# Performance work log

Measured on AMD Instinct MI355X. Metric: run time of the kernel, lower is better.

Reference implementation:

```python
import jax, jax.numpy as jnp
import numpy as np

N_VAR = 1_000_000
N_CON = 500_000
N_EDGE = 8_000_000
H = 10  # n_h_feats


def setup_inputs() -> dict:
    key = jax.random.key(0)
    ks = jax.random.split(key, 20)
    f32 = jnp.float32
    s = 0.3  # weight init scale
    return {
        'var_c': jax.random.normal(ks[0], (N_VAR,), f32),
        'var_x': jax.random.normal(ks[1], (N_VAR,), f32),
        'con_b': jax.random.normal(ks[2], (N_CON,), f32),
        'edge_src': jax.random.randint(ks[3], (N_EDGE,), 0, N_VAR, jnp.int32),
        'edge_dst': jax.random.randint(ks[4], (N_EDGE,), 0, N_CON, jnp.int32),
        'edge_w': jax.random.uniform(ks[5], (N_EDGE,), f32),
        'Wv': jax.random.normal(ks[6], (2, H), f32) * s,
        'bv': jnp.zeros((H,), f32),
        'Wc': jax.random.normal(ks[7], (1, H), f32) * s,
        'bc': jnp.zeros((H,), f32),
        'W1': jax.random.normal(ks[8], (H, H), f32) * s,
        'b1': jnp.zeros((H,), f32),
        'W2': jax.random.normal(ks[9], (H, H), f32) * s,
        'b2': jnp.zeros((H,), f32),
        'Wo1': jax.random.normal(ks[10], (H, H), f32) * s,
        'bo1': jnp.zeros((H,), f32),
        'Wo2': jax.random.normal(ks[11], (H, H), f32) * s,
        'bo2': jnp.zeros((H,), f32),
        'Wo3': jax.random.normal(ks[12], (H, 1), f32) * s,
        'bo3': jnp.zeros((1,), f32),
    }


def _graph_conv(feat_src, src, dst, w, n_dst, deg_src, deg_dst, W, b):
    # DGL GraphConv, norm='both', with edge weights:
    # h = D_src^{-1/2} x ; m_e = h[src_e] * w_e ; agg = scatter_sum(m, dst)
    # out = (D_dst^{-1/2} agg) @ W + b
    h = feat_src * jax.lax.rsqrt(deg_src)[:, None]
    m = h[src] * w[:, None]                      # [E, H] gather + scale
    agg = jax.ops.segment_sum(m, dst, num_segments=n_dst)  # scatter-add
    agg = agg * jax.lax.rsqrt(deg_dst)[:, None]
    return agg @ W + b


def reference(var_c, var_x, con_b, edge_src, edge_dst, edge_w,
              Wv, bv, Wc, bc, W1, b1, W2, b2, Wo1, bo1, Wo2, bo2, Wo3, bo3):
    # node embeddings
    var_feat = jnp.stack([var_c, var_x], axis=1)            # [N_VAR, 2]
    con_feat = con_b.reshape(-1, 1)                          # [N_CON, 1]
    X_var = jax.nn.relu(var_feat @ Wv + bv)                  # [N_VAR, H]
    X_con = jax.nn.relu(con_feat @ Wc + bc)                  # computed in original; unused by GraphConv (no dst-feat term)

    ones_e = jnp.ones((edge_src.shape[0],), jnp.float32)
    deg_var = jnp.maximum(jax.ops.segment_sum(ones_e, edge_src, num_segments=N_VAR), 1.0)
    deg_con = jnp.maximum(jax.ops.segment_sum(ones_e, edge_dst, num_segments=N_CON), 1.0)

    # conv1['con'] is overwritten by conv2['con'] in the original (v2c src feats are X_var both times)
    h_con = jax.nn.relu(_graph_conv(X_var, edge_src, edge_dst, edge_w, N_CON, deg_var, deg_con, W2, b2))
    # likewise conv1['var'] is overwritten by conv2['var'] (c2v src feats are h_con both times)
    h_var = jax.nn.relu(_graph_conv(h_con, edge_dst, edge_src, edge_w, N_VAR, deg_con, deg_var, W2, b2))

    z = jax.nn.relu(h_var @ Wo1 + bo1)
    z = jax.nn.relu(z @ Wo2 + bo2)
    logit = z @ Wo3 + bo3                                    # [N_VAR, 1]
    # dgl.readout_nodes(op='mean') over a single batched graph
    return jnp.mean(logit, axis=0, keepdims=True)            # [1, 1]
```

## Files before the change

### kernel.cpp

```cpp
#include <hip/hip_runtime.h>

#define NVAR 1000000
#define NCON 500000
#define EPB 8192
#define FCAP 4480


__global__ __launch_bounds__(256) void kA_hist2(const int4* __restrict__ src4,
                                                const int4* __restrict__ dst4,
                                                unsigned* __restrict__ bhV,
                                                unsigned* __restrict__ bhC,
                                                int ne4, int nblk) {
    __shared__ unsigned hv[1024], hc[1024];
    int tid = threadIdx.x, b = blockIdx.x;
    for (int t = tid; t < 1024; t += 256) { hv[t] = 0; hc[t] = 0; }
    __syncthreads();
    int beg = b * (EPB / 4), end = min(ne4, beg + (EPB / 4));
    for (int i = beg + tid; i < end; i += 256) {
        int4 s = src4[i];
        int4 d = dst4[i];
        atomicAdd(&hv[s.x >> 10], 1u); atomicAdd(&hv[s.y >> 10], 1u);
        atomicAdd(&hv[s.z >> 10], 1u); atomicAdd(&hv[s.w >> 10], 1u);
        atomicAdd(&hc[d.x >> 9], 1u);  atomicAdd(&hc[d.y >> 9], 1u);
        atomicAdd(&hc[d.z >> 9], 1u);  atomicAdd(&hc[d.w >> 9], 1u);
    }
    __syncthreads();
    for (int t = tid; t < 1024; t += 256) {
        bhV[(size_t)t * nblk + b] = hv[t];
        bhC[(size_t)t * nblk + b] = hc[t];
    }
}

__global__ __launch_bounds__(256) void kA_scat(const int* __restrict__ keys,
                                               const int* __restrict__ vals,
                                               const float* __restrict__ w,
                                               const unsigned int* __restrict__ scanned,
                                               int2* __restrict__ bucketed,
                                               int ne, int shift, int nblk) {
    __shared__ unsigned int h[1024];
    __shared__ unsigned int lb[1024];
    __shared__ unsigned int gb[1024];
    __shared__ unsigned int sc[256];
    __shared__ int2 stage[EPB];
    int tid = threadIdx.x, b = blockIdx.x;
    for (int t = tid; t < 1024; t += 256) {
        h[t] = 0;
        gb[t] = scanned[(size_t)t * nblk + b];
    }
    __syncthreads();
    int beg = b * EPB, end = min(ne, beg + EPB), cnt = end - beg;
    int cnt4 = cnt >> 2;
    const int4* keys4 = (const int4*)(keys + beg);
    for (int i = tid; i < cnt4; i += 256) {
        int4 k = keys4[i];
        atomicAdd(&h[k.x >> shift], 1u);
        atomicAdd(&h[k.y >> shift], 1u);
        atomicAdd(&h[k.z >> shift], 1u);
        atomicAdd(&h[k.w >> shift], 1u);
    }
    for (int i = cnt4 * 4 + tid; i < cnt; i += 256) atomicAdd(&h[keys[beg + i] >> shift], 1u);
    __syncthreads();
    unsigned v0, v1, v2, v3;
    int q = tid * 4;
    v0 = h[q]; v1 = h[q + 1]; v2 = h[q + 2]; v3 = h[q + 3];
    sc[tid] = v0 + v1 + v2 + v3;
    __syncthreads();
    for (int dd = 1; dd < 256; dd <<= 1) {
        unsigned add = (tid >= dd) ? sc[tid - dd] : 0u;
        __syncthreads();
        sc[tid] += add;
        __syncthreads();
    }
    unsigned ex = (tid == 0) ? 0u : sc[tid - 1];
    lb[q]     = ex;
    lb[q + 1] = ex + v0;
    lb[q + 2] = ex + v0 + v1;
    lb[q + 3] = ex + v0 + v1 + v2;
    __syncthreads();
    for (int t = tid; t < 1024; t += 256) h[t] = 0;
    __syncthreads();
    unsigned mask = (1u << shift) - 1u;
    const int4* vals4 = (const int4*)(vals + beg);
    const float4* w4 = (const float4*)(w + beg);
    for (int i = tid; i < cnt4; i += 256) {
        int4 k = keys4[i];
        int4 v = vals4[i];
        float4 ww = w4[i];
        {
            unsigned bkt = (unsigned)k.x >> shift;
            unsigned r = atomicAdd(&h[bkt], 1u);
            stage[lb[bkt] + r] = make_int2(__float_as_int(ww.x),
                                           (v.x << shift) | (unsigned)(k.x & (int)mask));
        }
        {
            unsigned bkt = (unsigned)k.y >> shift;
            unsigned r = atomicAdd(&h[bkt], 1u);
            stage[lb[bkt] + r] = make_int2(__float_as_int(ww.y),
                                           (v.y << shift) | (unsigned)(k.y & (int)mask));
        }
        {
            unsigned bkt = (unsigned)k.z >> shift;
            unsigned r = atomicAdd(&h[bkt], 1u);
            stage[lb[bkt] + r] = make_int2(__float_as_int(ww.z),
                                           (v.z << shift) | (unsigned)(k.z & (int)mask));
        }
        {
            unsigned bkt = (unsigned)k.w >> shift;
            unsigned r = atomicAdd(&h[bkt], 1u);
            stage[lb[bkt] + r] = make_int2(__float_as_int(ww.w),
                                           (v.w << shift) | (unsigned)(k.w & (int)mask));
        }
    }
    for (int i = cnt4 * 4 + tid; i < cnt; i += 256) {
        int k = keys[beg + i];
        unsigned bkt = (unsigned)k >> shift;
        unsigned r = atomicAdd(&h[bkt], 1u);
        stage[lb[bkt] + r] = make_int2(__float_as_int(w[beg + i]),
                                       (vals[beg + i] << shift) | (unsigned)(k & (int)mask));
    }
    __syncthreads();
    for (int i = tid; i < cnt; i += 256) {
        unsigned bb = 0;
#pragma unroll
        for (int step = 512; step > 0; step >>= 1) {
            unsigned cand = bb + step;
            if (cand < 1024 && lb[cand] <= (unsigned)i) bb = cand;
        }
        bucketed[gb[bb] + ((unsigned)i - lb[bb])] = stage[i];
    }
}

__global__ __launch_bounds__(256) void kB_degV(const int2* __restrict__ bucketed,
                                               const unsigned* __restrict__ scanned,
                                               unsigned* __restrict__ deg,
                                               int nnodes, int nblk) {
    __shared__ unsigned h[1024];
    int d = blockIdx.x, tid = threadIdx.x;
    unsigned base = scanned[(size_t)d * nblk], next = scanned[(size_t)(d + 1) * nblk];
    for (int t = tid; t < 1024; t += 256) h[t] = 0;
    __syncthreads();
    for (unsigned i = base + tid; i < next; i += 256)
        atomicAdd(&h[(unsigned)bucketed[i].y & 1023u], 1u);
    __syncthreads();
    int lo = d << 10;
    for (int t = tid; t < 1024; t += 256) {
        int node = lo + t;
        if (node < nnodes) deg[node] = h[t];
    }
}

__global__ __launch_bounds__(256) void k_scan_blocks(const unsigned int* __restrict__ in,
                                                     unsigned int* __restrict__ out,
                                                     unsigned int* __restrict__ bsum,
                                                     int n) {
    __shared__ unsigned int sT[256];
    int base = blockIdx.x * 1024 + threadIdx.x * 4;
    unsigned int v0 = 0, v1 = 0, v2 = 0, v3 = 0;
    if (base + 3 < n) {
        uint4 u = *(const uint4*)(in + base);
        v0 = u.x; v1 = u.y; v2 = u.z; v3 = u.w;
    } else {
        if (base     < n) v0 = in[base];
        if (base + 1 < n) v1 = in[base + 1];
        if (base + 2 < n) v2 = in[base + 2];
        if (base + 3 < n) v3 = in[base + 3];
    }
    sT[threadIdx.x] = v0 + v1 + v2 + v3;
    __syncthreads();
    for (int d = 1; d < 256; d <<= 1) {
        unsigned int add = (threadIdx.x >= (unsigned)d) ? sT[threadIdx.x - d] : 0u;
        __syncthreads();
        sT[threadIdx.x] += add;
        __syncthreads();
    }
    unsigned int excl = (threadIdx.x == 0) ? 0u : sT[threadIdx.x - 1];
    if (base     < n) out[base]     = excl;
    if (base + 1 < n) out[base + 1] = excl + v0;
    if (base + 2 < n) out[base + 2] = excl + v0 + v1;
    if (base + 3 < n) out[base + 3] = excl + v0 + v1 + v2;
    if (threadIdx.x == 255 && bsum) bsum[blockIdx.x] = sT[255];
}

__global__ __launch_bounds__(256) void k_scan_add(unsigned int* __restrict__ data,
                                                  const unsigned int* __restrict__ bscan,
                                                  int n) {
    int base = blockIdx.x * 1024 + threadIdx.x * 4;
    unsigned int add = bscan[blockIdx.x];
    if (base + 3 < n) {
        uint4 u = *(const uint4*)(data + base);
        u.x += add; u.y += add; u.z += add; u.w += add;
        *(uint4*)(data + base) = u;
    } else {
        if (base     < n) data[base]     += add;
        if (base + 1 < n) data[base + 1] += add;
        if (base + 2 < n) data[base + 2] += add;
        if (base + 3 < n) data[base + 3] += add;
    }
}


__global__ __launch_bounds__(256) void k_xvar_p(const float* __restrict__ var_c,
                                                const float* __restrict__ var_x,
                                                const unsigned int* __restrict__ deg_var,
                                                const float* __restrict__ Wv,
                                                const float* __restrict__ bv,
                                                float* __restrict__ Xs, int n) {
    int i = blockIdx.x * blockDim.x + threadIdx.x;
    if (i >= n) return;
    float c = var_c[i], x = var_x[i];
    float rs = rsqrtf(fmaxf((float)deg_var[i], 1.0f));
    float o[16];
#pragma unroll
    for (int j = 0; j < 10; j++) {
        float t = fmaf(c, Wv[j], fmaf(x, Wv[10 + j], bv[j]));
        o[j] = fmaxf(t, 0.0f) * rs;
    }
#pragma unroll
    for (int j = 10; j < 16; j++) o[j] = 0.0f;
    float4* dst4 = (float4*)(Xs + (size_t)i * 16);
#pragma unroll
    for (int j = 0; j < 4; j++)
        dst4[j] = make_float4(o[4 * j], o[4 * j + 1], o[4 * j + 2], o[4 * j + 3]);
}

#define GATHER4(eA, eB, eC, eD, TAB)                                          \
    {                                                                         \
        float4 v0 = *(const float4*)(TAB + (size_t)(eA).y * 16 + c0);         \
        float4 v1 = *(const float4*)(TAB + (size_t)(eB).y * 16 + c0);         \
        float4 v2 = *(const float4*)(TAB + (size_t)(eC).y * 16 + c0);         \
        float4 v3 = *(const float4*)(TAB + (size_t)(eD).y * 16 + c0);         \
        float w0 = __int_as_float((eA).x), w1 = __int_as_float((eB).x);       \
        float w2 = __int_as_float((eC).x), w3 = __int_as_float((eD).x);       \
        acc.x = fmaf(w0, v0.x, acc.x); acc.y = fmaf(w0, v0.y, acc.y);         \
        acc.z = fmaf(w0, v0.z, acc.z); acc.w = fmaf(w0, v0.w, acc.w);         \
        acc.x = fmaf(w1, v1.x, acc.x); acc.y = fmaf(w1, v1.y, acc.y);         \
        acc.z = fmaf(w1, v1.z, acc.z); acc.w = fmaf(w1, v1.w, acc.w);         \
        acc.x = fmaf(w2, v2.x, acc.x); acc.y = fmaf(w2, v2.y, acc.y);         \
        acc.z = fmaf(w2, v2.z, acc.z); acc.w = fmaf(w2, v2.w, acc.w);         \
        acc.x = fmaf(w3, v3.x, acc.x); acc.y = fmaf(w3, v3.y, acc.y);         \
        acc.z = fmaf(w3, v3.z, acc.z); acc.w = fmaf(w3, v3.w, acc.w);         \
    }

__global__ __launch_bounds__(512) void kF_con(const int2* __restrict__ bucketed,
                                              const unsigned* __restrict__ scanned,
                                              const float* __restrict__ Xs,
                                              const float* __restrict__ W2,
                                              const float* __restrict__ b2,
                                              float* __restrict__ hs, int nblk) {
    __shared__ unsigned h[512], s[512], tmp[512];
    __shared__ float sW[100], sb[10];
    __shared__ int2 stage[FCAP];
    int tid = threadIdx.x;
    int d = blockIdx.x >> 1, half = blockIdx.x & 1;
    for (int t = tid; t < 100; t += 512) sW[t] = W2[t];
    if (tid < 10) sb[tid] = b2[tid];
    h[tid] = 0;
    __syncthreads();
    unsigned base = scanned[(size_t)d * nblk];
    unsigned next = scanned[(size_t)(d + 1) * nblk];
    int bsz = (int)(next - base);
    for (int i = tid; i < bsz; i += 512)
        atomicAdd(&h[(unsigned)bucketed[base + i].y & 511u], 1u);
    __syncthreads();
    unsigned hv = h[tid];
    tmp[tid] = hv;
    __syncthreads();
    for (int dd = 1; dd < 512; dd <<= 1) {
        unsigned add = (tid >= dd) ? tmp[tid - dd] : 0u;
        __syncthreads();
        tmp[tid] += add;
        __syncthreads();
    }
    s[tid] = tmp[tid] - hv;
    __syncthreads();
    int hb = half * 256;
    unsigned own_beg = s[hb];
    unsigned own_end = (hb + 256 == 512) ? (unsigned)bsz : s[hb + 256];
    bool fit = (int)(own_end - own_beg) <= FCAP;
    h[tid] = 0;
    __syncthreads();
    if (fit) {
        for (int i = tid; i < bsz; i += 512) {
            int2 p = bucketed[base + i];
            unsigned low = (unsigned)p.y & 511u;
            if ((int)(low >> 8) == half) {
                unsigned r = atomicAdd(&h[low], 1u);
                stage[s[low] + r - own_beg] = make_int2(p.x, p.y >> 9);
            }
        }
    }
    __syncthreads();
    int quad = tid >> 2, lane = tid & 3, c0 = lane * 4;
#pragma unroll
    for (int rr = 0; rr < 2; rr++) {
        int node = hb + rr * 128 + quad;
        int g = (d << 9) + node;
        if (g >= NCON) continue;
        float4 acc = make_float4(0.f, 0.f, 0.f, 0.f);
        unsigned cnt;
        if (fit) {
            unsigned beg = s[node] - own_beg;
            cnt = h[node];
            unsigned end = beg + cnt, p = beg;
            for (; p + 4 <= end; p += 4) {
                int2 e0 = stage[p], e1 = stage[p + 1], e2 = stage[p + 2], e3 = stage[p + 3];
                GATHER4(e0, e1, e2, e3, Xs);
            }
            for (; p < end; ++p) {
                int2 e = stage[p];
                float4 v = *(const float4*)(Xs + (size_t)e.y * 16 + c0);
                float we = __int_as_float(e.x);
                acc.x = fmaf(we, v.x, acc.x); acc.y = fmaf(we, v.y, acc.y);
                acc.z = fmaf(we, v.z, acc.z); acc.w = fmaf(we, v.w, acc.w);
            }
        } else {
            cnt = 0;
            for (int i = 0; i < bsz; ++i) {
                int2 p = bucketed[base + i];
                if (((unsigned)p.y & 511u) == (unsigned)node) {
                    ++cnt;
                    float4 v = *(const float4*)(Xs + (size_t)((unsigned)p.y >> 9) * 16 + c0);
                    float we = __int_as_float(p.x);
                    acc.x = fmaf(we, v.x, acc.x); acc.y = fmaf(we, v.y, acc.y);
                    acc.z = fmaf(we, v.z, acc.z); acc.w = fmaf(we, v.w, acc.w);
                }
            }
        }
        float rs = rsqrtf(fmaxf((float)cnt, 1.0f));
        float a[10];
        a[0] = __shfl(acc.x, 0, 4); a[1] = __shfl(acc.y, 0, 4);
        a[2] = __shfl(acc.z, 0, 4); a[3] = __shfl(acc.w, 0, 4);
        a[4] = __shfl(acc.x, 1, 4); a[5] = __shfl(acc.y, 1, 4);
        a[6] = __shfl(acc.z, 1, 4); a[7] = __shfl(acc.w, 1, 4);
        a[8] = __shfl(acc.x, 2, 4); a[9] = __shfl(acc.y, 2, 4);
#pragma unroll
        for (int j = 0; j < 10; j++) a[j] *= rs;
        float o[12];
#pragma unroll
        for (int k = 0; k < 10; k++) {
            float t = sb[k];
#pragma unroll
            for (int j = 0; j < 10; j++) t = fmaf(a[j], sW[j * 10 + k], t);
            o[k] = fmaxf(t, 0.0f) * rs;
        }
        o[10] = 0.0f; o[11] = 0.0f;
        float4 wv = (lane < 3) ? make_float4(o[c0], o[c0 + 1], o[c0 + 2], o[c0 + 3])
                               : make_float4(0.f, 0.f, 0.f, 0.f);
        *(float4*)(hs + (size_t)g * 16 + c0) = wv;
    }
}

__global__ __launch_bounds__(512) void kF_fin(const int2* __restrict__ bucketed,
                                              const unsigned* __restrict__ scanned,
                                              const float* __restrict__ feat,
                                              const float* __restrict__ W2,
                                              const float* __restrict__ b2,
                                              const float* __restrict__ Wo1,
                                              const float* __restrict__ bo1,
                                              const float* __restrict__ Wo2,
                                              const float* __restrict__ bo2,
                                              const float* __restrict__ Wo3,
                                              const float* __restrict__ bo3,
                                              double* __restrict__ partials, int nblk) {
    __shared__ unsigned h[1024], s[1024], tmp[512];
    __shared__ float sW2[100], sb2[10], sWo1[100], sbo1[10], sWo2[100], sbo2[10], sWo3[10], sbo3v;
    __shared__ int2 stage[FCAP];
    __shared__ double red[512];
    int tid = threadIdx.x;
    int d = blockIdx.x >> 1, half = blockIdx.x & 1;
    for (int t = tid; t < 100; t += 512) { sW2[t] = W2[t]; sWo1[t] = Wo1[t]; sWo2[t] = Wo2[t]; }
    if (tid < 10) {
        sb2[tid] = b2[tid]; sbo1[tid] = bo1[tid]; sbo2[tid] = bo2[tid]; sWo3[tid] = Wo3[tid];
    }
    if (tid == 0) sbo3v = bo3[0];
    h[tid] = 0; h[tid + 512] = 0;
    __syncthreads();
    unsigned base = scanned[(size_t)d * nblk];
    unsigned next = scanned[(size_t)(d + 1) * nblk];
    int bsz = (int)(next - base);
    for (int i = tid; i < bsz; i += 512)
        atomicAdd(&h[(unsigned)bucketed[base + i].y & 1023u], 1u);
    __syncthreads();
    int q = tid * 2;
    unsigned v0 = h[q], v1 = h[q + 1];
    tmp[tid] = v0 + v1;
    __syncthreads();
    for (int dd = 1; dd < 512; dd <<= 1) {
        unsigned add = (tid >= dd) ? tmp[tid - dd] : 0u;
        __syncthreads();
        tmp[tid] += add;
        __syncthreads();
    }
    unsigned excl = tmp[tid] - (v0 + v1);
    s[q] = excl; s[q + 1] = excl + v0;
    __syncthreads();
    int hb = half * 512;
    unsigned own_beg = s[hb];
    unsigned own_end = (hb + 512 == 1024) ? (unsigned)bsz : s[hb + 512];
    bool fit = (int)(own_end - own_beg) <= FCAP;
    h[tid] = 0; h[tid + 512] = 0;
    __syncthreads();
    if (fit) {
        for (int i = tid; i < bsz; i += 512) {
            int2 p = bucketed[base + i];
            unsigned low = (unsigned)p.y & 1023u;
            if ((int)(low >> 9) == half) {
                unsigned r = atomicAdd(&h[low], 1u);
                stage[s[low] + r - own_beg] = make_int2(p.x, p.y >> 10);
            }
        }
    }
    __syncthreads();
    int quad = tid >> 2, lane = tid & 3, c0 = lane * 4;
    double accd = 0.0;
#pragma unroll
    for (int rr = 0; rr < 4; rr++) {
        int node = hb + rr * 128 + quad;
        int g = (d << 10) + node;
        if (g >= NVAR) continue;
        float4 acc = make_float4(0.f, 0.f, 0.f, 0.f);
        unsigned cnt;
        if (fit) {
            unsigned beg = s[node] - own_beg;
            cnt = h[node];
            unsigned end = beg + cnt, p = beg;
            for (; p + 4 <= end; p += 4) {
                int2 e0 = stage[p], e1 = stage[p + 1], e2 = stage[p + 2], e3 = stage[p + 3];
                GATHER4(e0, e1, e2, e3, feat);
            }
            for (; p < end; ++p) {
                int2 e = stage[p];
                float4 v = *(const float4*)(feat + (size_t)e.y * 16 + c0);
                float we = __int_as_float(e.x);
                acc.x = fmaf(we, v.x, acc.x); acc.y = fmaf(we, v.y, acc.y);
                acc.z = fmaf(we, v.z, acc.z); acc.w = fmaf(we, v.w, acc.w);
            }
        } else {
            cnt = 0;
            for (int i = 0; i < bsz; ++i) {
                int2 p = bucketed[base + i];
                if (((unsigned)p.y & 1023u) == (unsigned)node) {
                    ++cnt;
                    float4 v = *(const float4*)(feat + (size_t)((unsigned)p.y >> 10) * 16 + c0);
                    float we = __int_as_float(p.x);
                    acc.x = fmaf(we, v.x, acc.x); acc.y = fmaf(we, v.y, acc.y);
                    acc.z = fmaf(we, v.z, acc.z); acc.w = fmaf(we, v.w, acc.w);
                }
            }
        }
        float rs = rsqrtf(fmaxf((float)cnt, 1.0f));
        float a[10];
        a[0] = __shfl(acc.x, 0, 4); a[1] = __shfl(acc.y, 0, 4);
        a[2] = __shfl(acc.z, 0, 4); a[3] = __shfl(acc.w, 0, 4);
        a[4] = __shfl(acc.x, 1, 4); a[5] = __shfl(acc.y, 1, 4);
        a[6] = __shfl(acc.z, 1, 4); a[7] = __shfl(acc.w, 1, 4);
        a[8] = __shfl(acc.x, 2, 4); a[9] = __shfl(acc.y, 2, 4);
#pragma unroll
        for (int j = 0; j < 10; j++) a[j] *= rs;
        float hh[10], z[10];
#pragma unroll
        for (int k = 0; k < 10; k++) {
            float t = sb2[k];
#pragma unroll
            for (int j = 0; j < 10; j++) t = fmaf(a[j], sW2[j * 10 + k], t);
            hh[k] = fmaxf(t, 0.0f);
        }
#pragma unroll
        for (int k = 0; k < 10; k++) {
            float t = sbo1[k];
#pragma unroll
            for (int j = 0; j < 10; j++) t = fmaf(hh[j], sWo1[j * 10 + k], t);
            z[k] = fmaxf(t, 0.0f);
        }
        float t3 = sbo3v;
#pragma unroll
        for (int k = 0; k < 10; k++) {
            float t = sbo2[k];
#pragma unroll
            for (int j = 0; j < 10; j++) t = fmaf(z[j], sWo2[j * 10 + k], t);
            t = fmaxf(t, 0.0f);
            t3 = fmaf(t, sWo3[k], t3);
        }
        if (lane == 0) accd += (double)t3;
    }
    red[tid] = accd;
    __syncthreads();
    for (int off = 256; off > 0; off >>= 1) {
        if (tid < off) red[tid] += red[tid + off];
        __syncthreads();
    }
    if (tid == 0) partials[blockIdx.x] = red[0];
}

__global__ __launch_bounds__(256) void k_out(const double* __restrict__ partials, int np,
                                             float* __restrict__ out) {
    __shared__ double red[256];
    double a = 0.0;
    for (int i = threadIdx.x; i < np; i += blockDim.x) a += partials[i];
    red[threadIdx.x] = a;
    __syncthreads();
    for (int off = 128; off > 0; off >>= 1) {
        if (threadIdx.x < off) red[threadIdx.x] += red[threadIdx.x + off];
        __syncthreads();
    }
    if (threadIdx.x == 0) out[0] = (float)(red[0] / (double)NVAR);
}


extern "C" void kernel_launch(void* const* d_in, const int* in_sizes, int n_in,
                              void* d_out, int out_size, void* d_ws, size_t ws_size,
                              hipStream_t stream) {
    const float* var_c  = (const float*)d_in[0];
    const float* var_x  = (const float*)d_in[1];
    const int*   e_src  = (const int*)d_in[3];
    const int*   e_dst  = (const int*)d_in[4];
    const float* e_w    = (const float*)d_in[5];
    const float* Wv     = (const float*)d_in[6];
    const float* bv     = (const float*)d_in[7];
    const float* W2     = (const float*)d_in[12];
    const float* b2     = (const float*)d_in[13];
    const float* Wo1    = (const float*)d_in[14];
    const float* bo1    = (const float*)d_in[15];
    const float* Wo2    = (const float*)d_in[16];
    const float* bo2    = (const float*)d_in[17];
    const float* Wo3    = (const float*)d_in[18];
    const float* bo3    = (const float*)d_in[19];
    float* out = (float*)d_out;
    const int ne = in_sizes[3];
    (void)n_in; (void)out_size; (void)ws_size;

    const int B = 256;
    const int nblkA = (ne + EPB - 1) / EPB;
    const int scanN = 1024 * nblkA;
    const int NBs   = (scanN + 1023) / 1024;
    const int BKV   = (NVAR + 1023) >> 10;
    const int BKC   = (NCON + 511) >> 9;
    const int ne4   = ne / 4;

    char* ws = (char*)d_ws;
    size_t off = 0;
    auto walloc = [&](size_t bytes) {
        void* p = ws + off;
        off = (off + bytes + 255) & ~(size_t)255;
        return p;
    };

    int2*     bucketedV = (int2*)walloc((size_t)ne * 8);
    int2*     bucketedC = (int2*)walloc((size_t)ne * 8);
    float*    Xs64      = (float*)walloc((size_t)NVAR * 16 * 4);
    float*    hs64      = (float*)walloc((size_t)NCON * 16 * 4);
    unsigned* scannedV  = (unsigned*)walloc((size_t)scanN * 4);
    unsigned* scannedC  = (unsigned*)walloc((size_t)scanN * 4);
    unsigned* bhV       = (unsigned*)walloc((size_t)scanN * 4);
    unsigned* bhC       = (unsigned*)walloc((size_t)scanN * 4);
    unsigned* bsumV     = (unsigned*)walloc(4096);
    unsigned* bscanV    = (unsigned*)walloc(4096);
    unsigned* bsumC     = (unsigned*)walloc(4096);
    unsigned* bscanC    = (unsigned*)walloc(4096);
    unsigned* bdummy    = (unsigned*)walloc(256);
    unsigned* deg_var   = bhV;
    double*   partials  = (double*)bhC;

    kA_hist2<<<nblkA, B, 0, stream>>>((const int4*)e_src, (const int4*)e_dst,
                                      bhV, bhC, ne4, nblkA);

    k_scan_blocks<<<NBs, B, 0, stream>>>(bhV, scannedV, bsumV, scanN);
    k_scan_blocks<<<1,   B, 0, stream>>>(bsumV, bscanV, bdummy, NBs);
    k_scan_add   <<<NBs, B, 0, stream>>>(scannedV, bscanV, scanN);
    k_scan_blocks<<<NBs, B, 0, stream>>>(bhC, scannedC, bsumC, scanN);
    k_scan_blocks<<<1,   B, 0, stream>>>(bsumC, bscanC, bdummy, NBs);
    k_scan_add   <<<NBs, B, 0, stream>>>(scannedC, bscanC, scanN);

    kA_scat<<<nblkA, B, 0, stream>>>(e_src, e_dst, e_w, scannedV, bucketedV, ne, 10, nblkA);

    kB_degV<<<BKV, B, 0, stream>>>(bucketedV, scannedV, deg_var, NVAR, nblkA);

    k_xvar_p<<<(NVAR + B - 1) / B, B, 0, stream>>>(var_c, var_x, deg_var, Wv, bv, Xs64, NVAR);

    kA_scat<<<nblkA, B, 0, stream>>>(e_dst, e_src, e_w, scannedC, bucketedC, ne, 9, nblkA);

    kF_con<<<BKC * 2, 512, 0, stream>>>(bucketedC, scannedC, Xs64, W2, b2, hs64, nblkA);

    kF_fin<<<BKV * 2, 512, 0, stream>>>(bucketedV, scannedV, hs64, W2, b2,
                                        Wo1, bo1, Wo2, bo2, Wo3, bo3, partials, nblkA);

    k_out<<<1, B, 0, stream>>>(partials, BKV * 2, out);
}
```

Baseline: 580.0 us.

## Precompute per-node degree prefix sums globally instead of per-block histogram and scan

```diff
diff --git a/kernel.cpp b/kernel.cpp
--- a/kernel.cpp
+++ b/kernel.cpp
@@ -130,28 +130,30 @@
     }
 }
 
-__global__ __launch_bounds__(256) void kB_degV(const int2* __restrict__ bucketed,
-                                               const unsigned* __restrict__ scanned,
-                                               unsigned* __restrict__ deg,
-                                               int nnodes, int nblk) {
+__global__ __launch_bounds__(256) void kDeg(const int2* __restrict__ bucketed,
+                                            const unsigned* __restrict__ scanned,
+                                            unsigned* __restrict__ deg,
+                                            int nnodes, int nblk, int lowbits) {
     __shared__ unsigned h[1024];
     int d = blockIdx.x, tid = threadIdx.x;
+    int W = 1 << lowbits;
+    unsigned mask = (unsigned)(W - 1);
     unsigned base = scanned[(size_t)d * nblk], next = scanned[(size_t)(d + 1) * nblk];
-    for (int t = tid; t < 1024; t += 256) h[t] = 0;
+    for (int t = tid; t < W; t += 256) h[t] = 0;
     __syncthreads();
     for (unsigned i = base + tid; i < next; i += 256)
-        atomicAdd(&h[(unsigned)bucketed[i].y & 1023u], 1u);
-    __syncthreads();
-    int lo = d << 10;
-    for (int t = tid; t < 1024; t += 256) {
+        atomicAdd(&h[(unsigned)bucketed[i].y & mask], 1u);
+    __syncthreads();
+    int lo = d << lowbits;
+    for (int t = tid; t < W; t += 256) {
         int node = lo + t;
         if (node < nnodes) deg[node] = h[t];
     }
 }
 
-__global__ __launch_bounds__(256) void k_scan_blocks(const unsigned int* __restrict__ in,
-                                                     unsigned int* __restrict__ out,
-                                                     unsigned int* __restrict__ bsum,
+__global__ __launch_bounds__(256) void k_scan_blocks(const unsigned int* in,
+                                                     unsigned int* out,
+                                                     unsigned int* bsum,
                                                      int n) {
     __shared__ unsigned int sT[256];
     int base = blockIdx.x * 1024 + threadIdx.x * 4;
@@ -243,49 +245,38 @@
 
 __global__ __launch_bounds__(512) void kF_con(const int2* __restrict__ bucketed,
                                               const unsigned* __restrict__ scanned,
+                                              const unsigned* __restrict__ startC,
                                               const float* __restrict__ Xs,
                                               const float* __restrict__ W2,
                                               const float* __restrict__ b2,
-                                              float* __restrict__ hs, int nblk) {
-    __shared__ unsigned h[512], s[512], tmp[512];
+                                              float* __restrict__ hs, int nblk, int netot) {
+    __shared__ unsigned sraw[257], cr[256];
     __shared__ float sW[100], sb[10];
     __shared__ int2 stage[FCAP];
     int tid = threadIdx.x;
     int d = blockIdx.x >> 1, half = blockIdx.x & 1;
+    int gbase = (d << 9) + half * 256;
     for (int t = tid; t < 100; t += 512) sW[t] = W2[t];
     if (tid < 10) sb[tid] = b2[tid];
-    h[tid] = 0;
-    __syncthreads();
-    unsigned base = scanned[(size_t)d * nblk];
-    unsigned next = scanned[(size_t)(d + 1) * nblk];
-    int bsz = (int)(next - base);
-    for (int i = tid; i < bsz; i += 512)
-        atomicAdd(&h[(unsigned)bucketed[base + i].y & 511u], 1u);
-    __syncthreads();
-    unsigned hv = h[tid];
-    tmp[tid] = hv;
-    __syncthreads();
-    for (int dd = 1; dd < 512; dd <<= 1) {
-        unsigned add = (tid >= dd) ? tmp[tid - dd] : 0u;
-        __syncthreads();
-        tmp[tid] += add;
-        __syncthreads();
-    }
-    s[tid] = tmp[tid] - hv;
-    __syncthreads();
-    int hb = half * 256;
-    unsigned own_beg = s[hb];
-    unsigned own_end = (hb + 256 == 512) ? (unsigned)bsz : s[hb + 256];
+    for (int t = tid; t < 257; t += 512) {
+        int g = gbase + t;
+        sraw[t] = (g < NCON) ? startC[g] : (unsigned)netot;
+    }
+    if (tid < 256) cr[tid] = 0;
+    __syncthreads();
+    unsigned own_beg = sraw[0], own_end = sraw[256];
     bool fit = (int)(own_end - own_beg) <= FCAP;
-    h[tid] = 0;
-    __syncthreads();
+    unsigned bbase = scanned[(size_t)d * nblk];
+    unsigned bnext = scanned[(size_t)(d + 1) * nblk];
+    int bsz = (int)(bnext - bbase);
     if (fit) {
         for (int i = tid; i < bsz; i += 512) {
-            int2 p = bucketed[base + i];
+            int2 p = bucketed[bbase + i];
             unsigned low = (unsigned)p.y & 511u;
             if ((int)(low >> 8) == half) {
-                unsigned r = atomicAdd(&h[low], 1u);
-                stage[s[low] + r - own_beg] = make_int2(p.x, p.y >> 9);
+                unsigned nl = low & 255u;
+                unsigned r = atomicAdd(&cr[nl], 1u);
+                stage[sraw[nl] - own_beg + r] = make_int2(p.x, p.y >> 9);
             }
         }
     }
@@ -293,14 +284,14 @@
     int quad = tid >> 2, lane = tid & 3, c0 = lane * 4;
 #pragma unroll
     for (int rr = 0; rr < 2; rr++) {
-        int node = hb + rr * 128 + quad;
-        int g = (d << 9) + node;
+        int nl = rr * 128 + quad;
+        int g = gbase + nl;
         if (g >= NCON) continue;
         float4 acc = make_float4(0.f, 0.f, 0.f, 0.f);
         unsigned cnt;
         if (fit) {
-            unsigned beg = s[node] - own_beg;
-            cnt = h[node];
+            unsigned beg = sraw[nl] - own_beg;
+            cnt = cr[nl];
             unsigned end = beg + cnt, p = beg;
             for (; p + 4 <= end; p += 4) {
                 int2 e0 = stage[p], e1 = stage[p + 1], e2 = stage[p + 2], e3 = stage[p + 3];
@@ -315,9 +306,10 @@
             }
         } else {
             cnt = 0;
+            unsigned target = (unsigned)(half * 256 + nl);
             for (int i = 0; i < bsz; ++i) {
-                int2 p = bucketed[base + i];
-                if (((unsigned)p.y & 511u) == (unsigned)node) {
+                int2 p = bucketed[bbase + i];
+                if (((unsigned)p.y & 511u) == target) {
                     ++cnt;
                     float4 v = *(const float4*)(Xs + (size_t)((unsigned)p.y >> 9) * 16 + c0);
                     float we = __int_as_float(p.x);
@@ -352,6 +344,7 @@
 
 __global__ __launch_bounds__(512) void kF_fin(const int2* __restrict__ bucketed,
                                               const unsigned* __restrict__ scanned,
+                                              const unsigned* __restrict__ startV,
                                               const float* __restrict__ feat,
                                               const float* __restrict__ W2,
                                               const float* __restrict__ b2,
@@ -361,52 +354,38 @@
                                               const float* __restrict__ bo2,
                                               const float* __restrict__ Wo3,
                                               const float* __restrict__ bo3,
-                                              double* __restrict__ partials, int nblk) {
-    __shared__ unsigned h[1024], s[1024], tmp[512];
+                                              double* __restrict__ partials, int nblk, int netot) {
+    __shared__ unsigned sraw[513], cr[512];
     __shared__ float sW2[100], sb2[10], sWo1[100], sbo1[10], sWo2[100], sbo2[10], sWo3[10], sbo3v;
     __shared__ int2 stage[FCAP];
     __shared__ double red[512];
     int tid = threadIdx.x;
     int d = blockIdx.x >> 1, half = blockIdx.x & 1;
+    int gbase = (d << 10) + half * 512;
     for (int t = tid; t < 100; t += 512) { sW2[t] = W2[t]; sWo1[t] = Wo1[t]; sWo2[t] = Wo2[t]; }
     if (tid < 10) {
         sb2[tid] = b2[tid]; sbo1[tid] = bo1[tid]; sbo2[tid] = bo2[tid]; sWo3[tid] = Wo3[tid];
     }
     if (tid == 0) sbo3v = bo3[0];
-    h[tid] = 0; h[tid + 512] = 0;
-    __syncthreads();
-    unsigned base = scanned[(size_t)d * nblk];
-    unsigned next = scanned[(size_t)(d + 1) * nblk];
-    int bsz = (int)(next - base);
-    for (int i = tid; i < bsz; i += 512)
-        atomicAdd(&h[(unsigned)bucketed[base + i].y & 1023u], 1u);
-    __syncthreads();
-    int q = tid * 2;
-    unsigned v0 = h[q], v1 = h[q + 1];
-    tmp[tid] = v0 + v1;
-    __syncthreads();
-    for (int dd = 1; dd < 512; dd <<= 1) {
-        unsigned add = (tid >= dd) ? tmp[tid - dd] : 0u;
-        __syncthreads();
-        tmp[tid] += add;
-        __syncthreads();
-    }
-    unsigned excl = tmp[tid] - (v0 + v1);
-    s[q] = excl; s[q + 1] = excl + v0;
-    __syncthreads();
-    int hb = half * 512;
-    unsigned own_beg = s[hb];
-    unsigned own_end = (hb + 512 == 1024) ? (unsigned)bsz : s[hb + 512];
+    for (int t = tid; t < 513; t += 512) {
+        int g = gbase + t;
+        sraw[t] = (g < NVAR) ? startV[g] : (unsigned)netot;
+    }
+    cr[tid] = 0;
+    __syncthreads();
+    unsigned own_beg = sraw[0], own_end = sraw[512];
     bool fit = (int)(own_end - own_beg) <= FCAP;
-    h[tid] = 0; h[tid + 512] = 0;
-    __syncthreads();
+    unsigned bbase = scanned[(size_t)d * nblk];
+    unsigned bnext = scanned[(size_t)(d + 1) * nblk];
+    int bsz = (int)(bnext - bbase);
     if (fit) {
         for (int i = tid; i < bsz; i += 512) {
-            int2 p = bucketed[base + i];
+            int2 p = bucketed[bbase + i];
             unsigned low = (unsigned)p.y & 1023u;
             if ((int)(low >> 9) == half) {
-                unsigned r = atomicAdd(&h[low], 1u);
-                stage[s[low] + r - own_beg] = make_int2(p.x, p.y >> 10);
+                unsigned nl = low & 511u;
+                unsigned r = atomicAdd(&cr[nl], 1u);
+                stage[sraw[nl] - own_beg + r] = make_int2(p.x, p.y >> 10);
             }
         }
     }
@@ -415,14 +394,14 @@
     double accd = 0.0;
 #pragma unroll
     for (int rr = 0; rr < 4; rr++) {
-        int node = hb + rr * 128 + quad;
-        int g = (d << 10) + node;
+        int nl = rr * 128 + quad;
+        int g = gbase + nl;
         if (g >= NVAR) continue;
         float4 acc = make_float4(0.f, 0.f, 0.f, 0.f);
         unsigned cnt;
         if (fit) {
-            unsigned beg = s[node] - own_beg;
-            cnt = h[node];
+            unsigned beg = sraw[nl] - own_beg;
+            cnt = cr[nl];
             unsigned end = beg + cnt, p = beg;
             for (; p + 4 <= end; p += 4) {
                 int2 e0 = stage[p], e1 = stage[p + 1], e2 = stage[p + 2], e3 = stage[p + 3];
@@ -437,9 +416,10 @@
             }
         } else {
             cnt = 0;
+            unsigned target = (unsigned)(half * 512 + nl);
             for (int i = 0; i < bsz; ++i) {
-                int2 p = bucketed[base + i];
-                if (((unsigned)p.y & 1023u) == (unsigned)node) {
+                int2 p = bucketed[bbase + i];
+                if (((unsigned)p.y & 1023u) == target) {
                     ++cnt;
                     float4 v = *(const float4*)(feat + (size_t)((unsigned)p.y >> 10) * 16 + c0);
                     float we = __int_as_float(p.x);
@@ -535,6 +515,8 @@
     const int NBs   = (scanN + 1023) / 1024;
     const int BKV   = (NVAR + 1023) >> 10;
     const int BKC   = (NCON + 511) >> 9;
+    const int NBV   = (NVAR + 1023) / 1024;
+    const int NBC   = (NCON + 1023) / 1024;
     const int ne4   = ne / 4;
 
     char* ws = (char*)d_ws;
@@ -553,36 +535,45 @@
     unsigned* scannedC  = (unsigned*)walloc((size_t)scanN * 4);
     unsigned* bhV       = (unsigned*)walloc((size_t)scanN * 4);
     unsigned* bhC       = (unsigned*)walloc((size_t)scanN * 4);
-    unsigned* bsumV     = (unsigned*)walloc(4096);
-    unsigned* bscanV    = (unsigned*)walloc(4096);
-    unsigned* bsumC     = (unsigned*)walloc(4096);
-    unsigned* bscanC    = (unsigned*)walloc(4096);
+    unsigned* bsumA     = (unsigned*)walloc(4096);
+    unsigned* bscanA    = (unsigned*)walloc(4096);
     unsigned* bdummy    = (unsigned*)walloc(256);
+    double*   partials  = (double*)walloc((size_t)(BKV * 2) * 8 + 64);
     unsigned* deg_var   = bhV;
-    double*   partials  = (double*)bhC;
+    unsigned* deg_con   = bhC;
 
     kA_hist2<<<nblkA, B, 0, stream>>>((const int4*)e_src, (const int4*)e_dst,
                                       bhV, bhC, ne4, nblkA);
 
-    k_scan_blocks<<<NBs, B, 0, stream>>>(bhV, scannedV, bsumV, scanN);
-    k_scan_blocks<<<1,   B, 0, stream>>>(bsumV, bscanV, bdummy, NBs);
-    k_scan_add   <<<NBs, B, 0, stream>>>(scannedV, bscanV, scanN);
-    k_scan_blocks<<<NBs, B, 0, stream>>>(bhC, scannedC, bsumC, scanN);
-    k_scan_blocks<<<1,   B, 0, stream>>>(bsumC, bscanC, bdummy, NBs);
-    k_scan_add   <<<NBs, B, 0, stream>>>(scannedC, bscanC, scanN);
+    k_scan_blocks<<<NBs, B, 0, stream>>>(bhV, scannedV, bsumA, scanN);
+    k_scan_blocks<<<1,   B, 0, stream>>>(bsumA, bscanA, bdummy, NBs);
+    k_scan_add   <<<NBs, B, 0, stream>>>(scannedV, bscanA, scanN);
+    k_scan_blocks<<<NBs, B, 0, stream>>>(bhC, scannedC, bsumA, scanN);
+    k_scan_blocks<<<1,   B, 0, stream>>>(bsumA, bscanA, bdummy, NBs);
+    k_scan_add   <<<NBs, B, 0, stream>>>(scannedC, bscanA, scanN);
 
     kA_scat<<<nblkA, B, 0, stream>>>(e_src, e_dst, e_w, scannedV, bucketedV, ne, 10, nblkA);
 
-    kB_degV<<<BKV, B, 0, stream>>>(bucketedV, scannedV, deg_var, NVAR, nblkA);
+    kDeg<<<BKV, B, 0, stream>>>(bucketedV, scannedV, deg_var, NVAR, nblkA, 10);
 
     k_xvar_p<<<(NVAR + B - 1) / B, B, 0, stream>>>(var_c, var_x, deg_var, Wv, bv, Xs64, NVAR);
 
+    k_scan_blocks<<<NBV, B, 0, stream>>>(deg_var, deg_var, bsumA, NVAR);
+    k_scan_blocks<<<1,   B, 0, stream>>>(bsumA, bscanA, bdummy, NBV);
+    k_scan_add   <<<NBV, B, 0, stream>>>(deg_var, bscanA, NVAR);
+
     kA_scat<<<nblkA, B, 0, stream>>>(e_dst, e_src, e_w, scannedC, bucketedC, ne, 9, nblkA);
 
-    kF_con<<<BKC * 2, 512, 0, stream>>>(bucketedC, scannedC, Xs64, W2, b2, hs64, nblkA);
-
-    kF_fin<<<BKV * 2, 512, 0, stream>>>(bucketedV, scannedV, hs64, W2, b2,
-                                        Wo1, bo1, Wo2, bo2, Wo3, bo3, partials, nblkA);
+    kDeg<<<BKC, B, 0, stream>>>(bucketedC, scannedC, deg_con, NCON, nblkA, 9);
+    k_scan_blocks<<<NBC, B, 0, stream>>>(deg_con, deg_con, bsumA, NCON);
+    k_scan_blocks<<<1,   B, 0, stream>>>(bsumA, bscanA, bdummy, NBC);
+    k_scan_add   <<<NBC, B, 0, stream>>>(deg_con, bscanA, NCON);
+
+    kF_con<<<BKC * 2, 512, 0, stream>>>(bucketedC, scannedC, deg_con, Xs64, W2, b2,
+                                        hs64, nblkA, ne);
+
+    kF_fin<<<BKV * 2, 512, 0, stream>>>(bucketedV, scannedV, deg_var, hs64, W2, b2,
+                                        Wo1, bo1, Wo2, bo2, Wo3, bo3, partials, nblkA, ne);
 
     k_out<<<1, B, 0, stream>>>(partials, BKV * 2, out);
 }
```

Measured after the change: 585.5 us. About the same (+0.9%).
